# Optimization experiments

Hardware: AMD Instinct MI355X
Metric: run time of the kernel (lower is better)

The kernel has to match this reference:

```python
import jax, jax.numpy as jnp
import numpy as np

L = 2048      # target/source sequence length (self-attention)
N = 2         # batch size
E = 256       # embed_dim
H = 8         # num_heads
N_AGENTS = 16


def setup_inputs() -> dict:
    key = jax.random.key(0)
    ks = jax.random.split(key, 9)
    w = 0.02
    ids = jax.random.randint(ks[7], (L,), 0, N_AGENTS, dtype=jnp.int32)
    return {
        "query": jax.random.normal(ks[0], (L, N, E), dtype=jnp.float32),
        "in_proj_weight": jax.random.normal(ks[1], (3 * E, E), dtype=jnp.float32) * w,
        "in_proj_bias": jax.random.normal(ks[2], (3 * E,), dtype=jnp.float32) * w,
        "in_proj_weight_self": jax.random.normal(ks[3], (2 * E, E), dtype=jnp.float32) * w,
        "in_proj_bias_self": jax.random.normal(ks[4], (2 * E,), dtype=jnp.float32) * w,
        "out_proj_weight": jax.random.normal(ks[5], (E, E), dtype=jnp.float32) * w,
        "out_proj_bias": jax.random.normal(ks[6], (E,), dtype=jnp.float32) * w,
        "q_identities": ids,                # self-attention: same identities for q and k
        "k_identities": ids,
    }


def reference(query, in_proj_weight, in_proj_bias, in_proj_weight_self,
              in_proj_bias_self, out_proj_weight, out_proj_bias,
              q_identities, k_identities):
    tgt_len, bsz, embed_dim = query.shape
    head_dim = embed_dim // H
    scaling = jnp.asarray(head_dim, query.dtype) ** -0.5

    # combined in-projection (self-attention fast path), then chunk into q,k,v
    qkv = query @ in_proj_weight.T + in_proj_bias            # (L,N,3E)
    q, k, v = jnp.split(qkv, 3, axis=-1)
    qk_self = query @ in_proj_weight_self.T + in_proj_bias_self  # (L,N,2E)
    q_self, k_self = jnp.split(qk_self, 2, axis=-1)

    q = q * scaling
    q_self = q_self * scaling

    def to_heads(x):  # (L,N,E) -> (N*H, L, head_dim), matching torch view+transpose
        return x.reshape(tgt_len, bsz * H, head_dim).transpose(1, 0, 2)

    q, k, v, q_self, k_self = map(to_heads, (q, k, v, q_self, k_self))

    w_inter = jnp.einsum('bld,bsd->bls', q, k)           # (N*H, L, S)
    w_self = jnp.einsum('bld,bsd->bls', q_self, k_self)  # (N*H, L, S)

    # agent-aware mask: 1 where query/key identities match, broadcast over batch*heads
    mask = (k_identities[None, :] == q_identities[:, None]).astype(query.dtype)  # (L,S)
    attn_weights = w_inter * (1.0 - mask) + w_self * mask

    attn = jax.nn.softmax(attn_weights, axis=-1)
    out = jnp.einsum('bls,bsd->bld', attn, v)            # (N*H, L, head_dim)
    out = out.transpose(1, 0, 2).reshape(tgt_len, bsz, embed_dim)
    out = out @ out_proj_weight.T + out_proj_bias        # (L,N,E)
    return out
```

## Files before the change

### kernel.cpp

```cpp
#include <hip/hip_runtime.h>
#include <hip/hip_bf16.h>

typedef __attribute__((ext_vector_type(8))) short short8b;
typedef __attribute__((ext_vector_type(4))) float float4v;

static __device__ __forceinline__ unsigned short f2bf_bits(float f) {
  union { __hip_bfloat16 h; unsigned short u; } c;
  c.h = __float2bfloat16(f);
  return c.u;
}

__global__ __launch_bounds__(256) void cast_all(
    const float* __restrict__ q, const float* __restrict__ w1,
    const float* __restrict__ w2, const float* __restrict__ w3,
    __hip_bfloat16* __restrict__ Xb, __hip_bfloat16* __restrict__ Wb,
    __hip_bfloat16* __restrict__ Wob) {
  int i = blockIdx.x * blockDim.x + threadIdx.x;
  if (i >= 360448) return;
  const float* src; __hip_bfloat16* dst; int j;
  if (i < 262144)      { src = q;  dst = Xb;          j = i; }
  else if (i < 311296) { src = w1; dst = Wb;          j = i - 262144; }
  else if (i < 344064) { src = w2; dst = Wb + 196608; j = i - 311296; }
  else                 { src = w3; dst = Wob;         j = i - 344064; }
  float4 v = reinterpret_cast<const float4*>(src)[j];
  union { ushort4 u; __hip_bfloat16 h[4]; } o;
  o.h[0] = __float2bfloat16(v.x); o.h[1] = __float2bfloat16(v.y);
  o.h[2] = __float2bfloat16(v.z); o.h[3] = __float2bfloat16(v.w);
  reinterpret_cast<ushort4*>(dst)[j] = o.u;
}

__global__ __launch_bounds__(256) void proj_gemm(
    const __hip_bfloat16* __restrict__ Xb, const __hip_bfloat16* __restrict__ Wb,
    const float* __restrict__ bias, const float* __restrict__ bias_s,
    __hip_bfloat16* __restrict__ Qs, __hip_bfloat16* __restrict__ Kg,
    __hip_bfloat16* __restrict__ Vt, __hip_bfloat16* __restrict__ Qf,
    __hip_bfloat16* __restrict__ Kf) {
    __shared__ __hip_bfloat16 At[128][40];
    __shared__ __hip_bfloat16 Bt[64][40];
    const int tid = threadIdx.x;
    const int lane = tid & 63, w = tid >> 6;
    const int ln = lane & 15, kg = lane >> 4;
    const int wr = w >> 1, wc = w & 1;
    const int rowBase = blockIdx.y * 128;
    const int colBase = blockIdx.x * 64;
    const __hip_bfloat16* Wsrc = Wb + (size_t)colBase * 256;
    float4v acc[4][2] = {};

    for (int kt = 0; kt < 8; ++kt) {
        int cid = tid;
#pragma unroll
        for (int p = 0; p < 2; ++p, cid += 256) {
            int row = cid >> 2, c = cid & 3;
            *(short8b*)&At[row][c * 8] =
                *(const short8b*)&Xb[(size_t)(rowBase + row) * 256 + kt * 32 + c * 8];
        }
        {
            int row = tid >> 2, c = tid & 3;
            *(short8b*)&Bt[row][c * 8] =
                *(const short8b*)&Wsrc[(size_t)row * 256 + kt * 32 + c * 8];
        }
        __syncthreads();
        short8b a[4], b[2];
#pragma unroll
        for (int mi = 0; mi < 4; ++mi) a[mi] = *(const short8b*)&At[wr * 64 + mi * 16 + ln][kg * 8];
#pragma unroll
        for (int nj = 0; nj < 2; ++nj) b[nj] = *(const short8b*)&Bt[wc * 32 + nj * 16 + ln][kg * 8];
#pragma unroll
        for (int mi = 0; mi < 4; ++mi)
#pragma unroll
            for (int nj = 0; nj < 2; ++nj)
                acc[mi][nj] = __builtin_amdgcn_mfma_f32_16x16x32_bf16(a[mi], b[nj], acc[mi][nj], 0, 0, 0);
        __syncthreads();
    }

    const float scaling = 0.17677669529663687f * 1.4426950408889634f;
#pragma unroll
    for (int mi = 0; mi < 4; ++mi) {
#pragma unroll
        for (int nj = 0; nj < 2; ++nj) {
            int j = colBase + wc * 32 + nj * 16 + ln;
            float bj = (j < 768) ? bias[j] : bias_s[j - 768];
#pragma unroll
            for (int r = 0; r < 4; ++r) {
                int row = rowBase + wr * 64 + mi * 16 + kg * 4 + r;
                float val = acc[mi][nj][r] + bj;
                int l = row >> 1, n = row & 1;
                if (j < 256) {
                    int h = j >> 5, d = j & 31;
                    Qs[(((n << 3) + h) * 2048 + l) * 32 + d] = __float2bfloat16(val * scaling);
                } else if (j < 512) {
                    int e = j - 256, h = e >> 5, d = e & 31;
                    Kg[(((n << 3) + h) * 2048 + l) * 32 + d] = __float2bfloat16(val);
                } else if (j < 768) {
                    int e = j - 512, h = e >> 5, d = e & 31;
                    Vt[(((n << 3) + h) * 32 + d) * 2048 + l] = __float2bfloat16(val);
                } else if (j < 1024) {
                    int e = j - 768, h = e >> 5, d = e & 31;
                    Qf[(((n << 3) + h) * 2048 + l) * 32 + d] = __float2bfloat16(val * scaling);
                } else {
                    int e = j - 1024, h = e >> 5, d = e & 31;
                    Kf[(((n << 3) + h) * 2048 + l) * 32 + d] = __float2bfloat16(val);
                }
            }
        }
    }
}

__global__ __launch_bounds__(256, 2) void agent_attn(
    const __hip_bfloat16* __restrict__ Qs, const __hip_bfloat16* __restrict__ Kg,
    const __hip_bfloat16* __restrict__ Vt, const __hip_bfloat16* __restrict__ Qf,
    const __hip_bfloat16* __restrict__ Kf, const int* __restrict__ qid_g,
    const int* __restrict__ kid_g, __hip_bfloat16* __restrict__ POb,
    float* __restrict__ PL) {
  __shared__ __hip_bfloat16 Klds[2][64][40];
  __shared__ __hip_bfloat16 Kslds[2][64][40];
  __shared__ __hip_bfloat16 Vlds[2][32][72];

  const int tid = threadIdx.x;
  const int lane = tid & 63, w = tid >> 6;
  const int ln = lane & 15, kg = lane >> 4;

  const int flat = blockIdx.x;
  const int slot = flat >> 3;
  const int bh = ((flat & 7) << 1) | (slot & 1);
  const int rest = slot >> 1;
  const int qg = rest & 31, split = rest >> 5;
  const int q0 = qg * 64 + w * 16;
  const int kbase = split * 1024;

  const __hip_bfloat16* Qb  = Qs + (size_t)bh * 2048 * 32;
  const __hip_bfloat16* Qfb = Qf + (size_t)bh * 2048 * 32;
  const __hip_bfloat16* Kb  = Kg + (size_t)bh * 2048 * 32;
  const __hip_bfloat16* Ksb = Kf + (size_t)bh * 2048 * 32;
  const __hip_bfloat16* Vb  = Vt + (size_t)bh * 32 * 2048;

  const int krho = tid >> 2, kseg = tid & 3;
  const int ksub = krho >> 4, ki = krho & 15;
  const int gK = ((ki >> 2) << 3) + (ki & 3) + ((ksub & 1) << 5) + ((ksub >> 1) << 2);
  const int vrow = tid >> 3, vseg = tid & 7;

  short8b bQ  = *(const short8b*)&Qb [(q0 + ln) * 32 + kg * 8];
  short8b bQf = *(const short8b*)&Qfb[(q0 + ln) * 32 + kg * 8];
  const int qidq = qid_g[q0 + ln];

  float lacc = 0.f;
  float4v O0 = {0.f, 0.f, 0.f, 0.f}, O1 = {0.f, 0.f, 0.f, 0.f};

  {
    short8b rk = *(const short8b*)&Kb [(size_t)(kbase + gK) * 32 + kseg * 8];
    short8b rs = *(const short8b*)&Ksb[(size_t)(kbase + gK) * 32 + kseg * 8];
    short8b rv = *(const short8b*)&Vb [(size_t)vrow * 2048 + kbase + vseg * 8];
    *(short8b*)&Klds [0][krho][kseg * 8] = rk;
    *(short8b*)&Kslds[0][krho][kseg * 8] = rs;
    *(short8b*)&Vlds [0][vrow][vseg * 8] = rv;
  }
  __syncthreads();

  short8b rk, rs, rv;
#pragma unroll 1
  for (int t = 0; t < 16; ++t) {
    const int cur = t & 1;
    const int s0 = kbase + t * 64;
    if (t < 15) {
      const int s0n = s0 + 64;
      rk = *(const short8b*)&Kb [(size_t)(s0n + gK) * 32 + kseg * 8];
      rs = *(const short8b*)&Ksb[(size_t)(s0n + gK) * 32 + kseg * 8];
      rv = *(const short8b*)&Vb [(size_t)vrow * 2048 + s0n + vseg * 8];
    }
    const int* ip = kid_g + s0 + kg * 8;
    int4 t0 = *(const int4*)(ip);
    int4 t1 = *(const int4*)(ip + 32);
    int4 t2 = *(const int4*)(ip + 4);
    int4 t3 = *(const int4*)(ip + 36);
    int sd[4][4] = {{t0.x, t0.y, t0.z, t0.w}, {t1.x, t1.y, t1.z, t1.w},
                    {t2.x, t2.y, t2.z, t2.w}, {t3.x, t3.y, t3.z, t3.w}};

    short8b aK[4], aS[4], bV[2][2];
#pragma unroll
    for (int sub = 0; sub < 4; ++sub) {
      aK[sub] = *(const short8b*)&Klds [cur][sub * 16 + ln][kg * 8];
      aS[sub] = *(const short8b*)&Kslds[cur][sub * 16 + ln][kg * 8];
    }
#pragma unroll
    for (int kk = 0; kk < 2; ++kk)
#pragma unroll
      for (int dh = 0; dh < 2; ++dh)
        bV[kk][dh] = *(const short8b*)&Vlds[cur][dh * 16 + ln][kk * 32 + kg * 8];

    float4v ci[4], cs[4];
    float4v z = {0.f, 0.f, 0.f, 0.f};
    __builtin_amdgcn_s_setprio(1);
#pragma unroll
    for (int sub = 0; sub < 4; ++sub) {
      ci[sub] = __builtin_amdgcn_mfma_f32_16x16x32_bf16(aK[sub], bQ,  z, 0, 0, 0);
      cs[sub] = __builtin_amdgcn_mfma_f32_16x16x32_bf16(aS[sub], bQf, z, 0, 0, 0);
    }
    __builtin_amdgcn_s_setprio(0);
    float p[4][4];
#pragma unroll
    for (int sub = 0; sub < 4; ++sub)
#pragma unroll
      for (int r = 0; r < 4; ++r)
        p[sub][r] = exp2f((sd[sub][r] == qidq) ? cs[sub][r] : ci[sub][r]);
    float y0 = (p[0][0] + p[0][1]) + (p[0][2] + p[0][3]);
    float y1 = (p[1][0] + p[1][1]) + (p[1][2] + p[1][3]);
    float y2 = (p[2][0] + p[2][1]) + (p[2][2] + p[2][3]);
    float y3 = (p[3][0] + p[3][1]) + (p[3][2] + p[3][3]);
    lacc += (y0 + y1) + (y2 + y3);
    union { short8b v; unsigned short us[8]; } apk[2];
#pragma unroll
    for (int kk = 0; kk < 2; ++kk) {
      apk[kk].us[0] = f2bf_bits(p[kk][0]);     apk[kk].us[1] = f2bf_bits(p[kk][1]);
      apk[kk].us[2] = f2bf_bits(p[kk][2]);     apk[kk].us[3] = f2bf_bits(p[kk][3]);
      apk[kk].us[4] = f2bf_bits(p[kk + 2][0]); apk[kk].us[5] = f2bf_bits(p[kk + 2][1]);
      apk[kk].us[6] = f2bf_bits(p[kk + 2][2]); apk[kk].us[7] = f2bf_bits(p[kk + 2][3]);
    }
    __builtin_amdgcn_s_setprio(1);
#pragma unroll
    for (int kk = 0; kk < 2; ++kk) {
      O0 = __builtin_amdgcn_mfma_f32_16x16x32_bf16(apk[kk].v, bV[kk][0], O0, 0, 0, 0);
      O1 = __builtin_amdgcn_mfma_f32_16x16x32_bf16(apk[kk].v, bV[kk][1], O1, 0, 0, 0);
    }
    __builtin_amdgcn_s_setprio(0);

    if (t < 15) {
      *(short8b*)&Klds [cur ^ 1][krho][kseg * 8] = rk;
      *(short8b*)&Kslds[cur ^ 1][krho][kseg * 8] = rs;
      *(short8b*)&Vlds [cur ^ 1][vrow][vseg * 8] = rv;
    }
    __syncthreads();
  }

  float ps = lacc;
  ps += __shfl_xor(ps, 16);
  ps += __shfl_xor(ps, 32);
  __hip_bfloat16* pob = POb + (size_t)(split * 16 + bh) * 2048 * 32;
  float* plb = PL + (size_t)(split * 16 + bh) * 2048;
#pragma unroll
  for (int r = 0; r < 4; ++r) {
    int q = q0 + kg * 4 + r;
    pob[(size_t)q * 32 + ln]      = __float2bfloat16(O0[r]);
    pob[(size_t)q * 32 + 16 + ln] = __float2bfloat16(O1[r]);
  }
  if (kg == 0) plb[q0 + ln] = ps;
}

__global__ __launch_bounds__(256) void combine_splits(
    const __hip_bfloat16* __restrict__ POb, const float* __restrict__ PL,
    __hip_bfloat16* __restrict__ Ab) {
  const int blk = blockIdx.x;
  const int bh = blk >> 6;
  const int q = ((blk & 63) << 5) | (threadIdx.x >> 3);
  const int d4 = threadIdx.x & 7;
  const int n = bh >> 3, h = bh & 7;
  float L = PL[(size_t)bh * 2048 + q] + PL[(size_t)(16 + bh) * 2048 + q];
  float inv = 1.f / L;
  union { ushort4 u; __hip_bfloat16 hh[4]; } a0, a1, o;
  a0.u = *(const ushort4*)&POb[((size_t)bh * 2048 + q) * 32 + d4 * 4];
  a1.u = *(const ushort4*)&POb[((size_t)(16 + bh) * 2048 + q) * 32 + d4 * 4];
#pragma unroll
  for (int i = 0; i < 4; ++i)
    o.hh[i] = __float2bfloat16((__bfloat162float(a0.hh[i]) +
                                __bfloat162float(a1.hh[i])) * inv);
  *(ushort4*)&Ab[((size_t)q * 2 + n) * 256 + h * 32 + d4 * 4] = o.u;
}

__global__ __launch_bounds__(256) void out_gemm(
    const __hip_bfloat16* __restrict__ A, const __hip_bfloat16* __restrict__ Wob,
    const float* __restrict__ bias, float* __restrict__ out) {
    __shared__ __hip_bfloat16 At[64][40];
    __shared__ __hip_bfloat16 Bt[64][40];
    const int tid = threadIdx.x;
    const int lane = tid & 63, w = tid >> 6;
    const int ln = lane & 15, kg = lane >> 4;
    const int wr = w >> 1, wc = w & 1;
    const int rowBase = blockIdx.y * 64;
    const int colBase = blockIdx.x * 64;
    float4v acc[2][2] = {};

    for (int kt = 0; kt < 8; ++kt) {
        int row = tid >> 2, c = tid & 3;
        *(short8b*)&At[row][c * 8] =
            *(const short8b*)&A[(size_t)(rowBase + row) * 256 + kt * 32 + c * 8];
        *(short8b*)&Bt[row][c * 8] =
            *(const short8b*)&Wob[(size_t)(colBase + row) * 256 + kt * 32 + c * 8];
        __syncthreads();
        short8b a[2], b[2];
#pragma unroll
        for (int mi = 0; mi < 2; ++mi) a[mi] = *(const short8b*)&At[wr * 32 + mi * 16 + ln][kg * 8];
#pragma unroll
        for (int nj = 0; nj < 2; ++nj) b[nj] = *(const short8b*)&Bt[wc * 32 + nj * 16 + ln][kg * 8];
#pragma unroll
        for (int mi = 0; mi < 2; ++mi)
#pragma unroll
            for (int nj = 0; nj < 2; ++nj)
                acc[mi][nj] = __builtin_amdgcn_mfma_f32_16x16x32_bf16(a[mi], b[nj], acc[mi][nj], 0, 0, 0);
        __syncthreads();
    }

#pragma unroll
    for (int mi = 0; mi < 2; ++mi) {
#pragma unroll
        for (int nj = 0; nj < 2; ++nj) {
            int j = colBase + wc * 32 + nj * 16 + ln;
            float bj = bias[j];
#pragma unroll
            for (int r = 0; r < 4; ++r) {
                int row = rowBase + wr * 32 + mi * 16 + kg * 4 + r;
                out[row * 256 + j] = acc[mi][nj][r] + bj;
            }
        }
    }
}

extern "C" void kernel_launch(void* const* d_in, const int* in_sizes, int n_in,
                              void* d_out, int out_size, void* d_ws, size_t ws_size,
                              hipStream_t stream) {
    const float* query = (const float*)d_in[0];
    const float* W_in  = (const float*)d_in[1];
    const float* b_in  = (const float*)d_in[2];
    const float* W_s   = (const float*)d_in[3];
    const float* b_s   = (const float*)d_in[4];
    const float* W_o   = (const float*)d_in[5];
    const float* b_o   = (const float*)d_in[6];
    const int*   qids  = (const int*)d_in[7];
    const int*   kids  = (const int*)d_in[8];
    float* out = (float*)d_out;

    __hip_bfloat16* Qs  = (__hip_bfloat16*)d_ws;
    __hip_bfloat16* Kg  = Qs + 16 * 2048 * 32;
    __hip_bfloat16* Vt  = Kg + 16 * 2048 * 32;
    __hip_bfloat16* Qf  = Vt + 16 * 2048 * 32;
    __hip_bfloat16* Kf  = Qf + 16 * 2048 * 32;
    __hip_bfloat16* Ab  = Kf + 16 * 2048 * 32;
    __hip_bfloat16* Xb  = Ab + 4096 * 256;
    __hip_bfloat16* Wbf = Xb + 4096 * 256;
    __hip_bfloat16* Wob = Wbf + 1280 * 256;
    __hip_bfloat16* POb = Wob + 256 * 256;
    float* PL = (float*)(POb + (size_t)2 * 16 * 2048 * 32);

    cast_all<<<1408, 256, 0, stream>>>(query, W_in, W_s, W_o, Xb, Wbf, Wob);
    proj_gemm<<<dim3(20, 32), 256, 0, stream>>>(Xb, Wbf, b_in, b_s,
                                                Qs, Kg, Vt, Qf, Kf);
    agent_attn<<<1024, 256, 0, stream>>>(Qs, Kg, Vt, Qf, Kf, qids, kids, POb, PL);
    combine_splits<<<1024, 256, 0, stream>>>(POb, PL, Ab);
    out_gemm<<<dim3(4, 64), 256, 0, stream>>>(Ab, Wob, b_o, out);
}
```

Before: 60.02 us.

## Remove key split in attention and fold normalization into attention epilogue

The attention kernel no longer splits the key range into two halves with a separate combine kernel. Each block now loops over all 32 key tiles, normalizes its output by the row sum, which it fetches per row with a lane shuffle, and writes straight into the layout the output projection reads. This removes the partial-output and partial-sum buffers, their round trip through global memory, and one kernel launch. In exchange the grid is halved, so there is less parallelism and each block runs a longer serial loop.

New measurement: 61.90 us. 1.03x slower.

```diff
diff --git a/kernel.cpp b/kernel.cpp
--- a/kernel.cpp
+++ b/kernel.cpp
@@ -110,8 +110,7 @@
     const __hip_bfloat16* __restrict__ Qs, const __hip_bfloat16* __restrict__ Kg,
     const __hip_bfloat16* __restrict__ Vt, const __hip_bfloat16* __restrict__ Qf,
     const __hip_bfloat16* __restrict__ Kf, const int* __restrict__ qid_g,
-    const int* __restrict__ kid_g, __hip_bfloat16* __restrict__ POb,
-    float* __restrict__ PL) {
+    const int* __restrict__ kid_g, __hip_bfloat16* __restrict__ Ab) {
   __shared__ __hip_bfloat16 Klds[2][64][40];
   __shared__ __hip_bfloat16 Kslds[2][64][40];
   __shared__ __hip_bfloat16 Vlds[2][32][72];
@@ -123,10 +122,9 @@
   const int flat = blockIdx.x;
   const int slot = flat >> 3;
   const int bh = ((flat & 7) << 1) | (slot & 1);
-  const int rest = slot >> 1;
-  const int qg = rest & 31, split = rest >> 5;
+  const int qg = slot >> 1;
   const int q0 = qg * 64 + w * 16;
-  const int kbase = split * 1024;
+  const int n = bh >> 3, h = bh & 7;
 
   const __hip_bfloat16* Qb  = Qs + (size_t)bh * 2048 * 32;
   const __hip_bfloat16* Qfb = Qf + (size_t)bh * 2048 * 32;
@@ -147,9 +145,9 @@
   float4v O0 = {0.f, 0.f, 0.f, 0.f}, O1 = {0.f, 0.f, 0.f, 0.f};
 
   {
-    short8b rk = *(const short8b*)&Kb [(size_t)(kbase + gK) * 32 + kseg * 8];
-    short8b rs = *(const short8b*)&Ksb[(size_t)(kbase + gK) * 32 + kseg * 8];
-    short8b rv = *(const short8b*)&Vb [(size_t)vrow * 2048 + kbase + vseg * 8];
+    short8b rk = *(const short8b*)&Kb [(size_t)gK * 32 + kseg * 8];
+    short8b rs = *(const short8b*)&Ksb[(size_t)gK * 32 + kseg * 8];
+    short8b rv = *(const short8b*)&Vb [(size_t)vrow * 2048 + vseg * 8];
     *(short8b*)&Klds [0][krho][kseg * 8] = rk;
     *(short8b*)&Kslds[0][krho][kseg * 8] = rs;
     *(short8b*)&Vlds [0][vrow][vseg * 8] = rv;
@@ -158,10 +156,10 @@
 
   short8b rk, rs, rv;
 #pragma unroll 1
-  for (int t = 0; t < 16; ++t) {
+  for (int t = 0; t < 32; ++t) {
     const int cur = t & 1;
-    const int s0 = kbase + t * 64;
-    if (t < 15) {
+    const int s0 = t * 64;
+    if (t < 31) {
       const int s0n = s0 + 64;
       rk = *(const short8b*)&Kb [(size_t)(s0n + gK) * 32 + kseg * 8];
       rs = *(const short8b*)&Ksb[(size_t)(s0n + gK) * 32 + kseg * 8];
@@ -223,7 +221,7 @@
     }
     __builtin_amdgcn_s_setprio(0);
 
-    if (t < 15) {
+    if (t < 31) {
       *(short8b*)&Klds [cur ^ 1][krho][kseg * 8] = rk;
       *(short8b*)&Kslds[cur ^ 1][krho][kseg * 8] = rs;
       *(short8b*)&Vlds [cur ^ 1][vrow][vseg * 8] = rv;
@@ -234,35 +232,15 @@
   float ps = lacc;
   ps += __shfl_xor(ps, 16);
   ps += __shfl_xor(ps, 32);
-  __hip_bfloat16* pob = POb + (size_t)(split * 16 + bh) * 2048 * 32;
-  float* plb = PL + (size_t)(split * 16 + bh) * 2048;
+  float inv = 1.0f / ps;
 #pragma unroll
   for (int r = 0; r < 4; ++r) {
+    float s_r = __shfl(inv, kg * 4 + r);
     int q = q0 + kg * 4 + r;
-    pob[(size_t)q * 32 + ln]      = __float2bfloat16(O0[r]);
-    pob[(size_t)q * 32 + 16 + ln] = __float2bfloat16(O1[r]);
+    size_t rowo = ((size_t)q * 2 + n) * 256 + h * 32;
+    Ab[rowo + ln]      = __float2bfloat16(O0[r] * s_r);
+    Ab[rowo + 16 + ln] = __float2bfloat16(O1[r] * s_r);
   }
-  if (kg == 0) plb[q0 + ln] = ps;
-}
-
-__global__ __launch_bounds__(256) void combine_splits(
-    const __hip_bfloat16* __restrict__ POb, const float* __restrict__ PL,
-    __hip_bfloat16* __restrict__ Ab) {
-  const int blk = blockIdx.x;
-  const int bh = blk >> 6;
-  const int q = ((blk & 63) << 5) | (threadIdx.x >> 3);
-  const int d4 = threadIdx.x & 7;
-  const int n = bh >> 3, h = bh & 7;
-  float L = PL[(size_t)bh * 2048 + q] + PL[(size_t)(16 + bh) * 2048 + q];
-  float inv = 1.f / L;
-  union { ushort4 u; __hip_bfloat16 hh[4]; } a0, a1, o;
-  a0.u = *(const ushort4*)&POb[((size_t)bh * 2048 + q) * 32 + d4 * 4];
-  a1.u = *(const ushort4*)&POb[((size_t)(16 + bh) * 2048 + q) * 32 + d4 * 4];
-#pragma unroll
-  for (int i = 0; i < 4; ++i)
-    o.hh[i] = __float2bfloat16((__bfloat162float(a0.hh[i]) +
-                                __bfloat162float(a1.hh[i])) * inv);
-  *(ushort4*)&Ab[((size_t)q * 2 + n) * 256 + h * 32 + d4 * 4] = o.u;
 }
 
 __global__ __launch_bounds__(256) void out_gemm(
@@ -336,13 +314,10 @@
     __hip_bfloat16* Xb  = Ab + 4096 * 256;
     __hip_bfloat16* Wbf = Xb + 4096 * 256;
     __hip_bfloat16* Wob = Wbf + 1280 * 256;
-    __hip_bfloat16* POb = Wob + 256 * 256;
-    float* PL = (float*)(POb + (size_t)2 * 16 * 2048 * 32);
 
     cast_all<<<1408, 256, 0, stream>>>(query, W_in, W_s, W_o, Xb, Wbf, Wob);
     proj_gemm<<<dim3(20, 32), 256, 0, stream>>>(Xb, Wbf, b_in, b_s,
                                                 Qs, Kg, Vt, Qf, Kf);
-    agent_attn<<<1024, 256, 0, stream>>>(Qs, Kg, Vt, Qf, Kf, qids, kids, POb, PL);
-    combine_splits<<<1024, 256, 0, stream>>>(POb, PL, Ab);
+    agent_attn<<<512, 256, 0, stream>>>(Qs, Kg, Vt, Qf, Kf, qids, kids, Ab);
     out_gemm<<<dim3(4, 64), 256, 0, stream>>>(Ab, Wob, b_o, out);
 }
```
